# Kernel optimization log

Measured on AMD Instinct MI355X. Metric: run time of the kernel, lower is better.

## Reference

```python
import jax, jax.numpy as jnp
import numpy as np


def setup_inputs() -> dict:
    key = jax.random.key(0)
    kq, kk, kv = jax.random.split(key, 3)
    # transpose_batch_sequence=True layout: [seq, batch, heads, head_dim]
    query = jax.random.normal(kq, (2048, 2, 32, 128), dtype=jnp.float32)
    k = jax.random.normal(kk, (2048, 2, 8, 128), dtype=jnp.float32)
    v = jax.random.normal(kv, (2048, 2, 8, 128), dtype=jnp.float32)
    return {"query": query, "key": k, "value": v}


def reference(query, key, value):
    # scale_attn_logits=True
    head_dim = query.shape[-1]
    q = query / jnp.sqrt(jnp.asarray(head_dim, dtype=query.dtype))
    h_q, h_kv = q.shape[-2], key.shape[-2]
    group_size = h_q // h_kv
    # [q, b, h_kv, g, d]
    gq = q.reshape((*q.shape[:2], h_kv, group_size, q.shape[-1]))
    # scores: [b, h_kv, g, q, k]
    attn = jnp.einsum('qbhgd,kbhd->bhgqk', gq, key)
    attn = jax.nn.softmax(attn, axis=-1)
    # output: [q, b, h_kv, g, d] -> [q, b, h_q, d]
    out = jnp.einsum('bhgqk,kbhd->qbhgd', attn, value)
    return out.reshape(query.shape)
```

## Files before the change

### kernel.cpp

```cpp
#include <hip/hip_runtime.h>

#define SEQ   2048
#define NB    2
#define NHQ   32
#define NHKV  8
#define HD    128
#define QTILE 256
#define QW    32
#define KVB   64
#define NT    (SEQ / KVB)
#define SCALE 0.08838834764831845f
#define QSCALE (0.08838834764831845f * 1.4426950408889634f)
#define THRL2 11.5f

#define QSTRIDE (NB * NHQ * HD)
#define KSTRIDE (NB * NHKV * HD)

typedef float f32x4  __attribute__((ext_vector_type(4)));
typedef float f32x16 __attribute__((ext_vector_type(16)));
typedef __bf16 bf16x8 __attribute__((ext_vector_type(8)));
typedef unsigned short ushort8 __attribute__((ext_vector_type(8)));
typedef unsigned int u32;
typedef unsigned int u32x2 __attribute__((ext_vector_type(2)));
typedef unsigned int u32x4 __attribute__((ext_vector_type(4)));

__device__ __forceinline__ unsigned short f2bf(float f) {
    union { float f; unsigned u; } c; c.f = f;
    return (unsigned short)((c.u + 0x7fffu + ((c.u >> 16) & 1u)) >> 16);
}

__device__ __forceinline__ void gload_lds16(const unsigned short* g, unsigned short* l) {
    __builtin_amdgcn_global_load_lds((const __attribute__((address_space(1))) u32*)g,
                                     (__attribute__((address_space(3))) u32*)l, 16, 0, 0);
}

__device__ __forceinline__ float ex2(float x) {
#if __has_builtin(__builtin_amdgcn_exp2f)
    return __builtin_amdgcn_exp2f(x);
#else
    return exp2f(x);
#endif
}

__device__ __forceinline__ u32 cvtpk(float lo, float hi) {
    u32 r;
    asm("v_cvt_pk_bf16_f32 %0, %1, %2" : "=v"(r) : "v"(lo), "v"(hi));
    return r;
}

__device__ __forceinline__ void pl32swap(u32& a, u32& b) {
#if __has_builtin(__builtin_amdgcn_permlane32_swap)
    u32x2 r = __builtin_amdgcn_permlane32_swap(a, b, false, false);
    a = r.x; b = r.y;
#else
    asm("v_permlane32_swap_b32 %0, %1" : "+v"(a), "+v"(b));
#endif
}

template <int B>
__device__ __forceinline__ bf16x8 make_pa(const f32x16 p) {
    u32 w0 = cvtpk(p[B + 0], p[B + 1]);
    u32 w2 = cvtpk(p[B + 4], p[B + 5]);
    pl32swap(w0, w2);
    u32 w1 = cvtpk(p[B + 2], p[B + 3]);
    u32 w3 = cvtpk(p[B + 6], p[B + 7]);
    pl32swap(w1, w3);
    u32x4 v = {w0, w1, w2, w3};
    return __builtin_bit_cast(bf16x8, v);
}

__global__ __launch_bounds__(256) void conv_k(const float* __restrict__ K,
                                              unsigned short* __restrict__ Kws) {
    int idx = blockIdx.x * 256 + threadIdx.x;
    int c  = idx & 15;
    int s  = (idx >> 4) & 2047;
    int bh = idx >> 15;
    int cs = c ^ (s & 7);
    const float* src = K + ((size_t)s * 16 + bh) * 128 + cs * 8;
    float4 f0 = *(const float4*)src;
    float4 f1 = *(const float4*)(src + 4);
    ushort8 u;
    u[0] = f2bf(f0.x); u[1] = f2bf(f0.y); u[2] = f2bf(f0.z); u[3] = f2bf(f0.w);
    u[4] = f2bf(f1.x); u[5] = f2bf(f1.y); u[6] = f2bf(f1.z); u[7] = f2bf(f1.w);
    *(ushort8*)&Kws[((size_t)bh * 2048 + s) * 128 + c * 8] = u;
}

__global__ __launch_bounds__(256) void conv_v(const float* __restrict__ V,
                                              unsigned short* __restrict__ Vt) {
    __shared__ float tile[64][129];
    int t64 = blockIdx.x & 31;
    int bh  = blockIdx.x >> 5;
    int kv0 = t64 * 64;
#pragma unroll
    for (int i = 0; i < 8; ++i) {
        int f4 = i * 256 + threadIdx.x;
        int kv = f4 >> 5, d4 = (f4 & 31) * 4;
        float4 v = *(const float4*)(V + ((size_t)(kv0 + kv) * 16 + bh) * 128 + d4);
        tile[kv][d4] = v.x; tile[kv][d4 + 1] = v.y;
        tile[kv][d4 + 2] = v.z; tile[kv][d4 + 3] = v.w;
    }
    __syncthreads();
#pragma unroll
    for (int i = 0; i < 4; ++i) {
        int lin = i * 256 + threadIdx.x;
        int c = lin & 7, d = lin >> 3;
        int cs = c ^ (d & 7);
        ushort8 u;
#pragma unroll
        for (int j = 0; j < 8; ++j) u[j] = f2bf(tile[cs * 8 + j][d]);
        *(ushort8*)&Vt[((size_t)bh * 128 + d) * 2048 + kv0 + c * 8] = u;
    }
}

__global__ __launch_bounds__(512, 1)
void attn_fwd6(const float* __restrict__ Q, const unsigned short* __restrict__ Kws,
               const unsigned short* __restrict__ Vtws, float* __restrict__ O) {
    __shared__ __align__(16) unsigned char smemc[98304];

    const int tid  = threadIdx.x;
    const int w    = tid >> 6;
    const int lane = tid & 63;
    const int q31  = lane & 31;
    const int h    = lane >> 5;
    const int c7   = q31 & 7;

    const int bid   = blockIdx.x;
    const int hkv   = bid & 7;
    const int rest  = bid >> 3;
    const int g     = rest & 3;
    const int b     = (rest >> 2) & 1;
    const int qtile = rest >> 3;
    const int hq    = hkv * 4 + g;

    const int qrow = qtile * QTILE + w * QW + q31;

    bf16x8 qf[8];
    {
        const float* qp = Q + (size_t)qrow * QSTRIDE + b * (NHQ * HD) + hq * HD;
#pragma unroll
        for (int s = 0; s < 8; ++s) {
            const float* p = qp + (2 * s + h) * 8;
            float4 f0 = *(const float4*)(p);
            float4 f1 = *(const float4*)(p + 4);
            ushort8 u;
            u[0] = f2bf(f0.x * QSCALE); u[1] = f2bf(f0.y * QSCALE);
            u[2] = f2bf(f0.z * QSCALE); u[3] = f2bf(f0.w * QSCALE);
            u[4] = f2bf(f1.x * QSCALE); u[5] = f2bf(f1.y * QSCALE);
            u[6] = f2bf(f1.z * QSCALE); u[7] = f2bf(f1.w * QSCALE);
            qf[s] = __builtin_bit_cast(bf16x8, u);
        }
    }

    u32 kad[8], vad[4];
#pragma unroll
    for (int s = 0; s < 8; ++s)
        kad[s] = q31 * 256 + (((2 * s + h) ^ c7) << 4);
#pragma unroll
    for (int ks = 0; ks < 4; ++ks)
        vad[ks] = 49152 + q31 * 128 + (((2 * ks + h) ^ c7) << 4);

    f32x16 acc[4];
#pragma unroll
    for (int db = 0; db < 4; ++db) acc[db] = (f32x16)0.f;
    float mr = -3e38f, lsum = 0.f;

    const unsigned short* kbh = Kws  + (size_t)(b * 8 + hkv) * 2048 * 128;
    const unsigned short* vbh = Vtws + (size_t)(b * 8 + hkv) * 128 * 2048;

#define STAGE(sofb, tt) do {                                                           \
        const int kv0s = (tt) * KVB;                                                   \
        _Pragma("unroll")                                                              \
        for (int i_ = 0; i_ < 2; ++i_) {                                               \
            const int c_ = w * 2 + i_;                                                 \
            gload_lds16(kbh + (size_t)(kv0s + c_ * 4 + (lane >> 4)) * 128 + (lane & 15) * 8, \
                        (unsigned short*)(smemc + (sofb) + c_ * 1024));                \
            gload_lds16(vbh + (size_t)(c_ * 8 + (lane >> 3)) * 2048 + kv0s + (lane & 7) * 8, \
                        (unsigned short*)(smemc + 49152 + (sofb) + c_ * 1024));        \
        }                                                                              \
    } while (0)

    STAGE(0, 0);
    STAGE(16384, 1);
    int kof = 0;
    int sof = 32768;

    for (int t = 0; t < NT; ++t) {
        if (t < NT - 1) {
            asm volatile("s_waitcnt vmcnt(4)" ::: "memory");
        } else {
            asm volatile("s_waitcnt vmcnt(0)" ::: "memory");
        }
        __builtin_amdgcn_s_barrier();
        if (t + 2 < NT) STAGE(sof, t + 2);

        f32x16 sa0 = (f32x16)0.f, sa1 = (f32x16)0.f;
        __builtin_amdgcn_s_setprio(1);
#pragma unroll
        for (int s = 0; s < 8; ++s) {
            bf16x8 k0 = *(const bf16x8*)&smemc[kad[s] + kof];
            bf16x8 k1 = *(const bf16x8*)&smemc[kad[s] + kof + 8192];
            sa0 = __builtin_amdgcn_mfma_f32_32x32x16_bf16(k0, qf[s], sa0, 0, 0, 0);
            sa1 = __builtin_amdgcn_mfma_f32_32x32x16_bf16(k1, qf[s], sa1, 0, 0, 0);
        }
        __builtin_amdgcn_s_setprio(0);

        float m4[4];
#pragma unroll
        for (int r = 0; r < 4; ++r)
            m4[r] = fmaxf(fmaxf(fmaxf(sa0[r], sa0[r + 4]), fmaxf(sa0[r + 8], sa0[r + 12])),
                          fmaxf(fmaxf(sa1[r], sa1[r + 4]), fmaxf(sa1[r + 8], sa1[r + 12])));
        float tm = fmaxf(fmaxf(m4[0], m4[1]), fmaxf(m4[2], m4[3]));
        tm = fmaxf(tm, __shfl_xor(tm, 32));

        if (!__all(tm <= mr + THRL2)) {
            float mn   = fmaxf(mr, tm);
            float corr = ex2(mr - mn);
            lsum *= corr;
#pragma unroll
            for (int db = 0; db < 4; ++db)
#pragma unroll
                for (int r = 0; r < 16; ++r) acc[db][r] *= corr;
            mr = mn;
        }

#pragma unroll
        for (int r = 0; r < 16; ++r) sa0[r] = ex2(sa0[r] - mr);
#pragma unroll
        for (int r = 0; r < 16; ++r) sa1[r] = ex2(sa1[r] - mr);
        float s4[4];
#pragma unroll
        for (int r = 0; r < 4; ++r)
            s4[r] = (sa0[r] + sa0[r + 4]) + (sa0[r + 8] + sa0[r + 12]) +
                    (sa1[r] + sa1[r + 4]) + (sa1[r + 8] + sa1[r + 12]);
        float ps = (s4[0] + s4[1]) + (s4[2] + s4[3]);
        ps += __shfl_xor(ps, 32);
        lsum += ps;

        bf16x8 pa[4];
        pa[0] = make_pa<0>(sa0);
        pa[1] = make_pa<8>(sa0);
        pa[2] = make_pa<0>(sa1);
        pa[3] = make_pa<8>(sa1);

        __builtin_amdgcn_s_setprio(1);
#pragma unroll
        for (int db = 0; db < 4; ++db) {
#pragma unroll
            for (int ks = 0; ks < 4; ++ks) {
                bf16x8 vf = *(const bf16x8*)&smemc[vad[ks] + kof + db * 4096];
                acc[db] = __builtin_amdgcn_mfma_f32_32x32x16_bf16(vf, pa[ks], acc[db], 0, 0, 0);
            }
        }
        __builtin_amdgcn_s_setprio(0);

        kof = (kof == 32768) ? 0 : kof + 16384;
        sof = (sof == 32768) ? 0 : sof + 16384;
    }
#undef STAGE

    __syncthreads();
    float invl = 1.f / lsum;
    float* ep = (float*)(void*)smemc + w * 2176;
    const int qtb = qtile * QTILE + w * QW;
    float* ob = O + b * (NHQ * HD) + hq * HD;

#pragma unroll
    for (int pass = 0; pass < 2; ++pass) {
#pragma unroll
        for (int db2 = 0; db2 < 2; ++db2) {
            const int db = pass * 2 + db2;
#pragma unroll
            for (int r = 0; r < 16; ++r)
                ep[q31 * 68 + db2 * 32 + (r & 3) + 8 * (r >> 2) + 4 * h] = acc[db][r] * invl;
        }
        __syncthreads();
#pragma unroll
        for (int i = 0; i < 8; ++i) {
            const int row = i * 4 + (lane >> 4);
            const int f4  = lane & 15;
            float4 val = *(const float4*)&ep[row * 68 + f4 * 4];
            *(float4*)(ob + (size_t)(qtb + row) * QSTRIDE + pass * 64 + f4 * 4) = val;
        }
        __syncthreads();
    }
}

#define KPAD  136
#define VPAD  72
#define PPAD  72
__global__ __launch_bounds__(512, 2)
void attn_fwd(const float* __restrict__ Q, const float* __restrict__ K,
              const float* __restrict__ V, float* __restrict__ O) {
    __shared__ __align__(16) unsigned short kbuf[KVB * KPAD];
    __shared__ __align__(16) unsigned short vbuf[HD * VPAD];
    __shared__ __align__(16) unsigned short pbuf[8][16 * PPAD];

    const int tid = threadIdx.x;
    const int w = tid >> 6, lane = tid & 63;
    const int row16 = lane & 15, kg = lane >> 4;
    const int bid = blockIdx.x;
    const int qtile = bid & 7, g = (bid >> 3) & 3, b = (bid >> 5) & 1, hkv = bid >> 6;
    const int hq = hkv * 4 + g;
    const int qbase = qtile * 256 + w * 32;

    ushort8 qf[2][4];
#pragma unroll
    for (int s = 0; s < 2; ++s) {
        const int qrow = qbase + s * 16 + row16;
        const float* qp = Q + (size_t)qrow * QSTRIDE + b * (NHQ * HD) + hq * HD;
#pragma unroll
        for (int kk = 0; kk < 4; ++kk) {
            const float* p = qp + kk * 32 + kg * 8;
            float4 f0 = *(const float4*)(p);
            float4 f1 = *(const float4*)(p + 4);
            ushort8 u;
            u[0] = f2bf(f0.x * SCALE); u[1] = f2bf(f0.y * SCALE);
            u[2] = f2bf(f0.z * SCALE); u[3] = f2bf(f0.w * SCALE);
            u[4] = f2bf(f1.x * SCALE); u[5] = f2bf(f1.y * SCALE);
            u[6] = f2bf(f1.z * SCALE); u[7] = f2bf(f1.w * SCALE);
            qf[s][kk] = u;
        }
    }
    float m[2][4], lsum[2][4];
    f32x4 acco[2][8];
#pragma unroll
    for (int s = 0; s < 2; ++s)
#pragma unroll
        for (int r = 0; r < 4; ++r) { m[s][r] = -1e30f; lsum[s][r] = 0.f; }
#pragma unroll
    for (int s = 0; s < 2; ++s)
#pragma unroll
        for (int n = 0; n < 8; ++n) acco[s][n] = (f32x4)0.f;

    const float* kb0 = K + b * (NHKV * HD) + hkv * HD;
    const float* vb0 = V + b * (NHKV * HD) + hkv * HD;

    for (int kvt = 0; kvt < SEQ / KVB; ++kvt) {
        const int kv0 = kvt * KVB;
        __syncthreads();
        const float* kb = kb0 + (size_t)kv0 * KSTRIDE;
#pragma unroll
        for (int i = 0; i < 2; ++i) {
            int c = i * 512 + tid;
            int row = c >> 4, c8 = c & 15;
            const float* src = kb + (size_t)row * KSTRIDE + c8 * 8;
            float4 f0 = *(const float4*)(src);
            float4 f1 = *(const float4*)(src + 4);
            ushort8 u;
            u[0] = f2bf(f0.x); u[1] = f2bf(f0.y); u[2] = f2bf(f0.z); u[3] = f2bf(f0.w);
            u[4] = f2bf(f1.x); u[5] = f2bf(f1.y); u[6] = f2bf(f1.z); u[7] = f2bf(f1.w);
            *(ushort8*)&kbuf[row * KPAD + c8 * 8] = u;
        }
        const float* vb = vb0 + (size_t)kv0 * KSTRIDE;
#pragma unroll
        for (int i = 0; i < 4; ++i) {
            int f4i = i * 512 + tid;
            int kv = f4i >> 5, d0 = (f4i & 31) * 4;
            float4 v4 = *(const float4*)(vb + (size_t)kv * KSTRIDE + d0);
            vbuf[(d0 + 0) * VPAD + kv] = f2bf(v4.x);
            vbuf[(d0 + 1) * VPAD + kv] = f2bf(v4.y);
            vbuf[(d0 + 2) * VPAD + kv] = f2bf(v4.z);
            vbuf[(d0 + 3) * VPAD + kv] = f2bf(v4.w);
        }
        __syncthreads();

        f32x4 sa[2][4];
#pragma unroll
        for (int s = 0; s < 2; ++s)
#pragma unroll
            for (int n = 0; n < 4; ++n) sa[s][n] = (f32x4)0.f;
#pragma unroll
        for (int kk = 0; kk < 4; ++kk) {
#pragma unroll
            for (int n = 0; n < 4; ++n) {
                bf16x8 bfr = *(const bf16x8*)&kbuf[(n * 16 + row16) * KPAD + kk * 32 + kg * 8];
                sa[0][n] = __builtin_amdgcn_mfma_f32_16x16x32_bf16(
                    __builtin_bit_cast(bf16x8, qf[0][kk]), bfr, sa[0][n], 0, 0, 0);
                sa[1][n] = __builtin_amdgcn_mfma_f32_16x16x32_bf16(
                    __builtin_bit_cast(bf16x8, qf[1][kk]), bfr, sa[1][n], 0, 0, 0);
            }
        }
#pragma unroll
        for (int s = 0; s < 2; ++s) {
#pragma unroll
            for (int r = 0; r < 4; ++r) {
                float tm = fmaxf(fmaxf(sa[s][0][r], sa[s][1][r]), fmaxf(sa[s][2][r], sa[s][3][r]));
                tm = fmaxf(tm, __shfl_xor(tm, 1, 16));
                tm = fmaxf(tm, __shfl_xor(tm, 2, 16));
                tm = fmaxf(tm, __shfl_xor(tm, 4, 16));
                tm = fmaxf(tm, __shfl_xor(tm, 8, 16));
                float mn = fmaxf(m[s][r], tm);
                float corr = __expf(m[s][r] - mn);
                float ps = 0.f;
                int prow = kg * 4 + r;
#pragma unroll
                for (int n = 0; n < 4; ++n) {
                    float p = __expf(sa[s][n][r] - mn);
                    ps += p;
                    pbuf[w][prow * PPAD + n * 16 + row16] = f2bf(p);
                }
                ps += __shfl_xor(ps, 1, 16);
                ps += __shfl_xor(ps, 2, 16);
                ps += __shfl_xor(ps, 4, 16);
                ps += __shfl_xor(ps, 8, 16);
                lsum[s][r] = lsum[s][r] * corr + ps;
                m[s][r] = mn;
#pragma unroll
                for (int n8 = 0; n8 < 8; ++n8) acco[s][n8][r] *= corr;
            }
#pragma unroll
            for (int kk2 = 0; kk2 < 2; ++kk2) {
                bf16x8 pa = *(const bf16x8*)&pbuf[w][row16 * PPAD + kk2 * 32 + kg * 8];
#pragma unroll
                for (int n8 = 0; n8 < 8; ++n8) {
                    bf16x8 vf = *(const bf16x8*)&vbuf[(n8 * 16 + row16) * VPAD + kk2 * 32 + kg * 8];
                    acco[s][n8] = __builtin_amdgcn_mfma_f32_16x16x32_bf16(pa, vf, acco[s][n8], 0, 0, 0);
                }
            }
        }
    }
    float* ob = O + b * (NHQ * HD) + hq * HD;
#pragma unroll
    for (int s = 0; s < 2; ++s)
#pragma unroll
        for (int r = 0; r < 4; ++r) {
            float inv = 1.f / lsum[s][r];
            int qrow = qbase + s * 16 + kg * 4 + r;
            float* op = ob + (size_t)qrow * QSTRIDE;
#pragma unroll
            for (int n8 = 0; n8 < 8; ++n8)
                op[n8 * 16 + row16] = acco[s][n8][r] * inv;
        }
}

extern "C" void kernel_launch(void* const* d_in, const int* in_sizes, int n_in,
                              void* d_out, int out_size, void* d_ws, size_t ws_size,
                              hipStream_t stream) {
    (void)in_sizes; (void)n_in; (void)out_size;
    const float* Q = (const float*)d_in[0];
    const float* K = (const float*)d_in[1];
    const float* V = (const float*)d_in[2];
    float* Out = (float*)d_out;

    const size_t kv_elems = (size_t)16 * 2048 * 128;
    const size_t need = kv_elems * 2 * sizeof(unsigned short);

    if (ws_size >= need) {
        unsigned short* Kws = (unsigned short*)d_ws;
        unsigned short* Vt  = Kws + kv_elems;
        conv_k<<<dim3(2048), dim3(256), 0, stream>>>(K, Kws);
        conv_v<<<dim3(512), dim3(256), 0, stream>>>(V, Vt);
        attn_fwd6<<<dim3(512), dim3(512), 0, stream>>>(Q, Kws, Vt, Out);
    } else {
        attn_fwd<<<dim3(512), dim3(512), 0, stream>>>(Q, K, V, Out);
    }
}
```

Baseline: 174.3 us.

## Shrink attention blocks to 4 waves and 32-key tiles for higher occupancy

The main attention kernel moves from 512-thread blocks holding 256 queries and 64-key tiles to 256-thread blocks holding 128 queries and 32-key tiles, using half the shared memory. Launch bounds now allow three blocks per CU, and the grid doubles to 1024 blocks. The V transpose swizzle and the LDS addressing are rebuilt for 32-key granularity, and the row sum is now reduced across half-waves once at the end instead of every tile. The aim is better latency hiding through more resident waves and better CU fill, at the cost of twice as many barriers and loop iterations, and less MFMA work per barrier.

```diff
diff --git a/kernel.cpp b/kernel.cpp
--- a/kernel.cpp
+++ b/kernel.cpp
@@ -5,9 +5,9 @@
 #define NHQ   32
 #define NHKV  8
 #define HD    128
-#define QTILE 256
+#define QTILE 128
 #define QW    32
-#define KVB   64
+#define KVB   32
 #define NT    (SEQ / KVB)
 #define SCALE 0.08838834764831845f
 #define QSCALE (0.08838834764831845f * 1.4426950408889634f)
@@ -104,25 +104,25 @@
     for (int i = 0; i < 4; ++i) {
         int lin = i * 256 + threadIdx.x;
         int c = lin & 7, d = lin >> 3;
-        int cs = c ^ (d & 7);
+        int grp = c >> 2, cw = c & 3;
+        int cs = cw ^ (d & 3);
         ushort8 u;
 #pragma unroll
-        for (int j = 0; j < 8; ++j) u[j] = f2bf(tile[cs * 8 + j][d]);
-        *(ushort8*)&Vt[((size_t)bh * 128 + d) * 2048 + kv0 + c * 8] = u;
-    }
-}
-
-__global__ __launch_bounds__(512, 1)
-void attn_fwd6(const float* __restrict__ Q, const unsigned short* __restrict__ Kws,
+        for (int j = 0; j < 8; ++j) u[j] = f2bf(tile[grp * 32 + cs * 8 + j][d]);
+        *(ushort8*)&Vt[((size_t)bh * 128 + d) * 2048 + kv0 + grp * 32 + cw * 8] = u;
+    }
+}
+
+__global__ __launch_bounds__(256, 3)
+void attn_fwd7(const float* __restrict__ Q, const unsigned short* __restrict__ Kws,
                const unsigned short* __restrict__ Vtws, float* __restrict__ O) {
-    __shared__ __align__(16) unsigned char smemc[98304];
+    __shared__ __align__(16) unsigned char smemc[49152];
 
     const int tid  = threadIdx.x;
     const int w    = tid >> 6;
     const int lane = tid & 63;
     const int q31  = lane & 31;
     const int h    = lane >> 5;
-    const int c7   = q31 & 7;
 
     const int bid   = blockIdx.x;
     const int hkv   = bid & 7;
@@ -151,13 +151,13 @@
         }
     }
 
-    u32 kad[8], vad[4];
+    u32 kad[8], vad[2];
 #pragma unroll
     for (int s = 0; s < 8; ++s)
-        kad[s] = q31 * 256 + (((2 * s + h) ^ c7) << 4);
-#pragma unroll
-    for (int ks = 0; ks < 4; ++ks)
-        vad[ks] = 49152 + q31 * 128 + (((2 * ks + h) ^ c7) << 4);
+        kad[s] = q31 * 256 + (((2 * s + h) ^ (q31 & 7)) << 4);
+#pragma unroll
+    for (int ks = 0; ks < 2; ++ks)
+        vad[ks] = 24576 + q31 * 64 + (((2 * ks + h) ^ (q31 & 3)) << 4);
 
     f32x16 acc[4];
 #pragma unroll
@@ -174,15 +174,15 @@
             const int c_ = w * 2 + i_;                                                 \
             gload_lds16(kbh + (size_t)(kv0s + c_ * 4 + (lane >> 4)) * 128 + (lane & 15) * 8, \
                         (unsigned short*)(smemc + (sofb) + c_ * 1024));                \
-            gload_lds16(vbh + (size_t)(c_ * 8 + (lane >> 3)) * 2048 + kv0s + (lane & 7) * 8, \
-                        (unsigned short*)(smemc + 49152 + (sofb) + c_ * 1024));        \
+            gload_lds16(vbh + (size_t)(c_ * 16 + (lane >> 2)) * 2048 + kv0s + (lane & 3) * 8, \
+                        (unsigned short*)(smemc + 24576 + (sofb) + c_ * 1024));        \
         }                                                                              \
     } while (0)
 
     STAGE(0, 0);
-    STAGE(16384, 1);
+    STAGE(8192, 1);
     int kof = 0;
-    int sof = 32768;
+    int sof = 16384;
 
     for (int t = 0; t < NT; ++t) {
         if (t < NT - 1) {
@@ -193,72 +193,63 @@
         __builtin_amdgcn_s_barrier();
         if (t + 2 < NT) STAGE(sof, t + 2);
 
-        f32x16 sa0 = (f32x16)0.f, sa1 = (f32x16)0.f;
+        f32x16 sa = (f32x16)0.f;
         __builtin_amdgcn_s_setprio(1);
 #pragma unroll
         for (int s = 0; s < 8; ++s) {
-            bf16x8 k0 = *(const bf16x8*)&smemc[kad[s] + kof];
-            bf16x8 k1 = *(const bf16x8*)&smemc[kad[s] + kof + 8192];
-            sa0 = __builtin_amdgcn_mfma_f32_32x32x16_bf16(k0, qf[s], sa0, 0, 0, 0);
-            sa1 = __builtin_amdgcn_mfma_f32_32x32x16_bf16(k1, qf[s], sa1, 0, 0, 0);
+            bf16x8 kf = *(const bf16x8*)&smemc[kad[s] + kof];
+            sa = __builtin_amdgcn_mfma_f32_32x32x16_bf16(kf, qf[s], sa, 0, 0, 0);
         }
         __builtin_amdgcn_s_setprio(0);
 
-        float m4[4];
-#pragma unroll
-        for (int r = 0; r < 4; ++r)
-            m4[r] = fmaxf(fmaxf(fmaxf(sa0[r], sa0[r + 4]), fmaxf(sa0[r + 8], sa0[r + 12])),
-                          fmaxf(fmaxf(sa1[r], sa1[r + 4]), fmaxf(sa1[r + 8], sa1[r + 12])));
-        float tm = fmaxf(fmaxf(m4[0], m4[1]), fmaxf(m4[2], m4[3]));
-        tm = fmaxf(tm, __shfl_xor(tm, 32));
-
-        if (!__all(tm <= mr + THRL2)) {
-            float mn   = fmaxf(mr, tm);
-            float corr = ex2(mr - mn);
-            lsum *= corr;
-#pragma unroll
-            for (int db = 0; db < 4; ++db)
-#pragma unroll
-                for (int r = 0; r < 16; ++r) acc[db][r] *= corr;
-            mr = mn;
-        }
-
-#pragma unroll
-        for (int r = 0; r < 16; ++r) sa0[r] = ex2(sa0[r] - mr);
-#pragma unroll
-        for (int r = 0; r < 16; ++r) sa1[r] = ex2(sa1[r] - mr);
-        float s4[4];
-#pragma unroll
-        for (int r = 0; r < 4; ++r)
-            s4[r] = (sa0[r] + sa0[r + 4]) + (sa0[r + 8] + sa0[r + 12]) +
-                    (sa1[r] + sa1[r + 4]) + (sa1[r + 8] + sa1[r + 12]);
-        float ps = (s4[0] + s4[1]) + (s4[2] + s4[3]);
-        ps += __shfl_xor(ps, 32);
-        lsum += ps;
-
-        bf16x8 pa[4];
-        pa[0] = make_pa<0>(sa0);
-        pa[1] = make_pa<8>(sa0);
-        pa[2] = make_pa<0>(sa1);
-        pa[3] = make_pa<8>(sa1);
+        {
+            float t0 = fmaxf(fmaxf(sa[0], sa[1]),   fmaxf(sa[2], sa[3]));
+            float t1 = fmaxf(fmaxf(sa[4], sa[5]),   fmaxf(sa[6], sa[7]));
+            float t2 = fmaxf(fmaxf(sa[8], sa[9]),   fmaxf(sa[10], sa[11]));
+            float t3 = fmaxf(fmaxf(sa[12], sa[13]), fmaxf(sa[14], sa[15]));
+            float tm = fmaxf(fmaxf(t0, t1), fmaxf(t2, t3));
+            tm = fmaxf(tm, __shfl_xor(tm, 32));
+            if (!__all(tm <= mr + THRL2)) {
+                float mn   = fmaxf(mr, tm);
+                float corr = ex2(mr - mn);
+                lsum *= corr;
+#pragma unroll
+                for (int db = 0; db < 4; ++db)
+#pragma unroll
+                    for (int r = 0; r < 16; ++r) acc[db][r] *= corr;
+                mr = mn;
+            }
+#pragma unroll
+            for (int r = 0; r < 16; ++r) sa[r] = ex2(sa[r] - mr);
+            float s0 = (sa[0] + sa[1]) + (sa[2] + sa[3]);
+            float s1 = (sa[4] + sa[5]) + (sa[6] + sa[7]);
+            float s2 = (sa[8] + sa[9]) + (sa[10] + sa[11]);
+            float s3 = (sa[12] + sa[13]) + (sa[14] + sa[15]);
+            lsum += (s0 + s1) + (s2 + s3);
+        }
+
+        bf16x8 pa[2];
+        pa[0] = make_pa<0>(sa);
+        pa[1] = make_pa<8>(sa);
 
         __builtin_amdgcn_s_setprio(1);
 #pragma unroll
         for (int db = 0; db < 4; ++db) {
 #pragma unroll
-            for (int ks = 0; ks < 4; ++ks) {
-                bf16x8 vf = *(const bf16x8*)&smemc[vad[ks] + kof + db * 4096];
+            for (int ks = 0; ks < 2; ++ks) {
+                bf16x8 vf = *(const bf16x8*)&smemc[vad[ks] + kof + db * 2048];
                 acc[db] = __builtin_amdgcn_mfma_f32_32x32x16_bf16(vf, pa[ks], acc[db], 0, 0, 0);
             }
         }
         __builtin_amdgcn_s_setprio(0);
 
-        kof = (kof == 32768) ? 0 : kof + 16384;
-        sof = (sof == 32768) ? 0 : sof + 16384;
+        kof = (kof == 16384) ? 0 : kof + 8192;
+        sof = (sof == 16384) ? 0 : sof + 8192;
     }
 #undef STAGE
 
     __syncthreads();
+    lsum += __shfl_xor(lsum, 32);
     float invl = 1.f / lsum;
     float* ep = (float*)(void*)smemc + w * 2176;
     const int qtb = qtile * QTILE + w * QW;
@@ -291,7 +282,7 @@
 __global__ __launch_bounds__(512, 2)
 void attn_fwd(const float* __restrict__ Q, const float* __restrict__ K,
               const float* __restrict__ V, float* __restrict__ O) {
-    __shared__ __align__(16) unsigned short kbuf[KVB * KPAD];
+    __shared__ __align__(16) unsigned short kbuf[64 * KPAD];
     __shared__ __align__(16) unsigned short vbuf[HD * VPAD];
     __shared__ __align__(16) unsigned short pbuf[8][16 * PPAD];
 
@@ -335,8 +326,8 @@
     const float* kb0 = K + b * (NHKV * HD) + hkv * HD;
     const float* vb0 = V + b * (NHKV * HD) + hkv * HD;
 
-    for (int kvt = 0; kvt < SEQ / KVB; ++kvt) {
-        const int kv0 = kvt * KVB;
+    for (int kvt = 0; kvt < SEQ / 64; ++kvt) {
+        const int kv0 = kvt * 64;
         __syncthreads();
         const float* kb = kb0 + (size_t)kv0 * KSTRIDE;
 #pragma unroll
@@ -450,7 +441,7 @@
         unsigned short* Vt  = Kws + kv_elems;
         conv_k<<<dim3(2048), dim3(256), 0, stream>>>(K, Kws);
         conv_v<<<dim3(512), dim3(256), 0, stream>>>(V, Vt);
-        attn_fwd6<<<dim3(512), dim3(512), 0, stream>>>(Q, Kws, Vt, Out);
+        attn_fwd7<<<dim3(1024), dim3(256), 0, stream>>>(Q, Kws, Vt, Out);
     } else {
         attn_fwd<<<dim3(512), dim3(512), 0, stream>>>(Q, K, V, Out);
     }
```

Measured after the change: 187.8 us. +7.7%, slower.
